# Kernel tuning notes

Measured on AMD Instinct MI355X. Metric: run time of the kernel, lower is better.

The kernel has to match this reference:

```python
import jax, jax.numpy as jnp
import numpy as np

NUM_LEVELS = 16
BASE_RES = 16
DESIRED_RES = 512
EMBED_C = 2
LOG2_HASHMAP = 19
N_POINTS = 262144


def _level_params():
    # torch-ngp gridencoder math, align_corners=True
    S = np.log2(DESIRED_RES / BASE_RES) / (NUM_LEVELS - 1)
    scales = np.exp2(np.arange(NUM_LEVELS) * S) * BASE_RES - 1.0  # float per-level scale
    res = np.ceil(scales).astype(np.int64) + 1                     # per-level grid resolution
    sizes = np.minimum(res ** 3, 2 ** LOG2_HASHMAP)
    sizes = ((sizes + 7) // 8) * 8                                 # round up to multiple of 8
    offsets = np.concatenate([[0], np.cumsum(sizes)])
    return scales.astype(np.float32), res.astype(np.int32), offsets.astype(np.int32)


_CORNERS = np.array([[(c >> d) & 1 for d in range(3)] for c in range(8)], dtype=np.int32)  # [8,3]


def _grid_encode(x, table):
    # x: [N,3] in [0,1]; table: [total_entries, EMBED_C]
    scales, res, offsets = _level_params()
    scales_j = jnp.asarray(scales)[:, None, None]                    # [L,1,1]
    res_j = jnp.asarray(res)[:, None, None]                          # [L,1,1]
    hsize = jnp.asarray(offsets[1:] - offsets[:-1])[:, None, None]   # [L,1,1]
    off = jnp.asarray(offsets[:-1])[:, None, None]                   # [L,1,1]
    pos = x[None, :, :] * scales_j                                   # [L,N,3]
    pos_floor = jnp.floor(pos)
    frac = pos - pos_floor                                           # [L,N,3]
    base = pos_floor.astype(jnp.int32)                               # [L,N,3]
    stride = jnp.concatenate([jnp.ones_like(res_j), res_j, res_j * res_j], axis=-1)  # [L,1,3]
    corners = jnp.asarray(_CORNERS)                                  # [8,3]
    cg = base[:, :, None, :] + corners[None, None]                   # [L,N,8,3]
    w = jnp.where(corners[None, None].astype(bool), frac[:, :, None, :], 1.0 - frac[:, :, None, :])
    w = w[..., 0] * w[..., 1] * w[..., 2]                            # [L,N,8] trilinear weights
    lin = jnp.sum(cg * stride[:, :, None, :], axis=-1)               # [L,N,8] linear corner index
    idx = off + lin % hsize                                          # tiled gridtype: modulo, no hash
    feats = table[idx]                                               # [L,N,8,C] gather
    out = jnp.einsum('lnk,lnkc->lnc', w, feats)                      # [L,N,C]
    n = out.shape[1]
    return out.transpose(1, 0, 2).reshape(n, NUM_LEVELS * EMBED_C)   # [N, L*C]


def setup_inputs() -> dict:
    key = jax.random.key(0)
    ks = jax.random.split(key, 8)
    _, _, offsets = _level_params()
    total = int(offsets[-1])
    inputcoords = jax.random.uniform(ks[0], (N_POINTS, 1, 3), dtype=jnp.float32)  # in [0,1): (x+1)/2 stays in [0,1]
    embeddings = jax.random.normal(ks[1], (total, 1, EMBED_C), dtype=jnp.float32) * 1e-2
    d_in = NUM_LEVELS * EMBED_C  # 32
    W0 = jax.random.normal(ks[2], (d_in, 32), dtype=jnp.float32) / np.sqrt(d_in)
    b0 = jnp.zeros((32,), jnp.float32)
    W1 = jax.random.normal(ks[3], (32, 32), dtype=jnp.float32) / np.sqrt(32.0)
    b1 = jnp.zeros((32,), jnp.float32)
    W2 = jax.random.normal(ks[4], (32, 1), dtype=jnp.float32) / np.sqrt(32.0)
    b2 = jnp.zeros((1,), jnp.float32)
    return {"inputcoords": inputcoords, "embeddings": embeddings,
            "W0": W0, "b0": b0, "W1": W1, "b1": b1, "W2": W2, "b2": b2}


def reference(inputcoords, embeddings, W0, b0, W1, b1, W2, b2):
    bound = 1.0
    x = ((inputcoords + bound) / (2.0 * bound)).reshape(-1, 3)       # [N,3]
    enc = _grid_encode(x, embeddings[:, 0])                          # [N, 32]
    h = enc.reshape(-1, 1, NUM_LEVELS * EMBED_C)                     # [N,1,32]
    h = jax.nn.leaky_relu(h @ W0 + b0, 0.01)
    h = jax.nn.leaky_relu(h @ W1 + b1, 0.01)
    return h @ W2 + b2                                               # [N,1,1]
```

## Files before the change

### kernel.cpp

```cpp
#include <hip/hip_runtime.h>

#define NLVL 16
#define NPTS_PER_BLOCK 256

constexpr float SCALEC[NLVL] = {
    15.0f, 19.15873679831797f, 24.39841683149119f, 31.0f,
    39.31747359663594f, 49.79683366298238f, 63.0f, 79.63494719327189f,
    100.59366732596477f, 127.0f, 160.26989438654376f, 202.18733465192954f,
    255.0f, 321.5397887730875f, 405.3746693038591f, 511.0f
};
constexpr int RESC[NLVL] = {
    16, 21, 26, 32, 41, 51, 64, 81, 102, 128, 162, 204, 256, 323, 407, 512
};
constexpr int OFFC[NLVL] = {
    0, 4096, 13360, 30936, 63704, 132632, 265288, 527432,
    1051720, 1576008, 2100296, 2624584, 3148872, 3673160, 4197448, 4721736
};
constexpr int HMASK = 0x7FFFF;

template<int L>
__device__ __forceinline__ void level_issue(float x, float y, float z,
                                            const float* __restrict__ emb,
                                            float4& q00, float4& q10,
                                            float4& q01, float4& q11,
                                            int& wmask)
{
    constexpr float s = SCALEC[L];
    constexpr int   r = RESC[L];
    constexpr int   off = OFFC[L];

    const float px = x * s, py = y * s, pz = z * s;
    const int bx = (int)floorf(px), by = (int)floorf(py), bz = (int)floorf(pz);
    const int lin = bx + r * by + r * r * bz;

    int i00 = lin, i10 = lin + r, i01 = lin + r * r, i11 = lin + r * r + r;
    if constexpr (L >= 7) {
        i00 &= HMASK; i10 &= HMASK; i01 &= HMASK; i11 &= HMASK;
        wmask = (i00 == HMASK ? 1 : 0) | (i10 == HMASK ? 2 : 0)
              | (i01 == HMASK ? 4 : 0) | (i11 == HMASK ? 8 : 0);
    } else {
        wmask = 0;
    }
    __builtin_memcpy(&q00, emb + 2 * (off + i00), 16);
    __builtin_memcpy(&q10, emb + 2 * (off + i10), 16);
    __builtin_memcpy(&q01, emb + 2 * (off + i01), 16);
    __builtin_memcpy(&q11, emb + 2 * (off + i11), 16);
}

template<int L>
__device__ __forceinline__ void level_accum(float x, float y, float z,
                                            const float* __restrict__ emb,
                                            float4 q00, float4 q10,
                                            float4 q01, float4 q11,
                                            int wmask,
                                            float* __restrict__ h0,
                                            const float* __restrict__ W0)
{
    constexpr float s = SCALEC[L];
    constexpr int   off = OFFC[L];

    const float px = x * s, py = y * s, pz = z * s;
    const float tx = px - floorf(px), ty = py - floorf(py), tz = pz - floorf(pz);

    if constexpr (L >= 7) {
        const float f0x = emb[2 * off], f0y = emb[2 * off + 1];
        q00.z = (wmask & 1) ? f0x : q00.z;  q00.w = (wmask & 1) ? f0y : q00.w;
        q10.z = (wmask & 2) ? f0x : q10.z;  q10.w = (wmask & 2) ? f0y : q10.w;
        q01.z = (wmask & 4) ? f0x : q01.z;  q01.w = (wmask & 4) ? f0y : q01.w;
        q11.z = (wmask & 8) ? f0x : q11.z;  q11.w = (wmask & 8) ? f0y : q11.w;
    }

    const float wx1 = tx, wx0 = 1.0f - tx;
    const float wy1 = ty, wy0 = 1.0f - ty;
    const float wz1 = tz, wz0 = 1.0f - tz;
    const float w00 = wy0 * wz0, w10 = wy1 * wz0;
    const float w01 = wy0 * wz1, w11 = wy1 * wz1;
    float a0 = 0.0f, a1 = 0.0f;
    a0 = fmaf(w00 * wx0, q00.x, a0); a1 = fmaf(w00 * wx0, q00.y, a1);
    a0 = fmaf(w00 * wx1, q00.z, a0); a1 = fmaf(w00 * wx1, q00.w, a1);
    a0 = fmaf(w10 * wx0, q10.x, a0); a1 = fmaf(w10 * wx0, q10.y, a1);
    a0 = fmaf(w10 * wx1, q10.z, a0); a1 = fmaf(w10 * wx1, q10.w, a1);
    a0 = fmaf(w01 * wx0, q01.x, a0); a1 = fmaf(w01 * wx0, q01.y, a1);
    a0 = fmaf(w01 * wx1, q01.z, a0); a1 = fmaf(w01 * wx1, q01.w, a1);
    a0 = fmaf(w11 * wx0, q11.x, a0); a1 = fmaf(w11 * wx0, q11.y, a1);
    a0 = fmaf(w11 * wx1, q11.z, a0); a1 = fmaf(w11 * wx1, q11.w, a1);

#pragma unroll
    for (int j = 0; j < 32; ++j)
        h0[j] = fmaf(a0, W0[(2 * L + 0) * 32 + j], h0[j]);
#pragma unroll
    for (int j = 0; j < 32; ++j)
        h0[j] = fmaf(a1, W0[(2 * L + 1) * 32 + j], h0[j]);
}

__global__ __launch_bounds__(NPTS_PER_BLOCK, 4)
void hashgrid_mlp_kernel(const float* __restrict__ coords,
                         const float* __restrict__ emb,
                         const float* __restrict__ W0,
                         const float* __restrict__ b0,
                         const float* __restrict__ W1,
                         const float* __restrict__ b1,
                         const float* __restrict__ W2,
                         const float* __restrict__ b2,
                         float* __restrict__ out,
                         int n)
{
    const int tid = blockIdx.x * blockDim.x + threadIdx.x;
    if (tid >= n) return;

    const float x = (coords[tid * 3 + 0] + 1.0f) * 0.5f;
    const float y = (coords[tid * 3 + 1] + 1.0f) * 0.5f;
    const float z = (coords[tid * 3 + 2] + 1.0f) * 0.5f;

    float h0[32];
#pragma unroll
    for (int j = 0; j < 32; ++j) h0[j] = b0[j];

    float4 a00, a10, a01, a11; int am;
    float4 b00, b10, b01, b11; int bm;
    float4 c00, c10, c01, c11; int cm;
    float4 d00, d10, d01, d11; int dm;

#define ISS(S, L) level_issue<L>(x, y, z, emb, S##00, S##10, S##01, S##11, S##m);
#define ACC(S, L) level_accum<L>(x, y, z, emb, S##00, S##10, S##01, S##11, S##m, h0, W0);

    ISS(a, 0) ISS(b, 1) ISS(c, 2) ISS(d, 3)
    ACC(a, 0)  ISS(a, 4)
    ACC(b, 1)  ISS(b, 5)
    ACC(c, 2)  ISS(c, 6)
    ACC(d, 3)  ISS(d, 7)
    ACC(a, 4)  ISS(a, 8)
    ACC(b, 5)  ISS(b, 9)
    ACC(c, 6)  ISS(c, 10)
    ACC(d, 7)  ISS(d, 11)
    ACC(a, 8)  ISS(a, 12)
    ACC(b, 9)  ISS(b, 13)
    ACC(c, 10) ISS(c, 14)
    ACC(d, 11) ISS(d, 15)
    ACC(a, 12)
    ACC(b, 13)
    ACC(c, 14)
    ACC(d, 15)

#undef ISS
#undef ACC

#pragma unroll
    for (int j = 0; j < 32; ++j) h0[j] = (h0[j] >= 0.0f) ? h0[j] : 0.01f * h0[j];

    float h1[32];
#pragma unroll
    for (int j = 0; j < 32; ++j) h1[j] = b1[j];
#pragma unroll
    for (int i = 0; i < 32; ++i) {
        const float e = h0[i];
#pragma unroll
        for (int j = 0; j < 32; ++j) h1[j] = fmaf(e, W1[i * 32 + j], h1[j]);
    }
#pragma unroll
    for (int j = 0; j < 32; ++j) h1[j] = (h1[j] >= 0.0f) ? h1[j] : 0.01f * h1[j];

    float acc = b2[0];
#pragma unroll
    for (int j = 0; j < 32; ++j) acc = fmaf(h1[j], W2[j], acc);

    out[tid] = acc;
}

extern "C" void kernel_launch(void* const* d_in, const int* in_sizes, int n_in,
                              void* d_out, int out_size, void* d_ws, size_t ws_size,
                              hipStream_t stream) {
    const float* coords = (const float*)d_in[0];
    const float* emb    = (const float*)d_in[1];
    const float* W0     = (const float*)d_in[2];
    const float* b0     = (const float*)d_in[3];
    const float* W1     = (const float*)d_in[4];
    const float* b1     = (const float*)d_in[5];
    const float* W2     = (const float*)d_in[6];
    const float* b2     = (const float*)d_in[7];
    float* out = (float*)d_out;

    const int n = in_sizes[0] / 3;
    const int blocks = (n + NPTS_PER_BLOCK - 1) / NPTS_PER_BLOCK;
    hashgrid_mlp_kernel<<<blocks, NPTS_PER_BLOCK, 0, stream>>>(
        coords, emb, W0, b0, W1, b1, W2, b2, out, n);
}
```

Before: 98.71 us.

## Issue embedding gathers via inline asm with explicit vmcnt waits for prefetch

Replaces the compiler-generated embedding loads with inline global_load_dwordx4 instructions and inserts explicit s_waitcnt vmcnt counters plus sched barriers. The goal is to keep four levels of gathers in flight, since the compiler might otherwise serialize the loads or wait too early. It risks correctness problems: the level_accum path also issues loads (emb[2*off] and W0 reads) that the compiler does not count, so the hand-set vmcnt values may not match. The sched barriers also restrict instruction scheduling.

After: 133.0 us. 34.8% more time.

```diff
diff --git a/kernel.cpp b/kernel.cpp
--- a/kernel.cpp
+++ b/kernel.cpp
@@ -1,4 +1,6 @@
 #include <hip/hip_runtime.h>
+
+typedef __attribute__((ext_vector_type(4))) float f32x4;
 
 #define NLVL 16
 #define NPTS_PER_BLOCK 256
@@ -21,8 +23,8 @@
 template<int L>
 __device__ __forceinline__ void level_issue(float x, float y, float z,
                                             const float* __restrict__ emb,
-                                            float4& q00, float4& q10,
-                                            float4& q01, float4& q11,
+                                            f32x4& q0, f32x4& q1,
+                                            f32x4& q2, f32x4& q3,
                                             int& wmask)
 {
     constexpr float s = SCALEC[L];
@@ -30,28 +32,31 @@
     constexpr int   off = OFFC[L];
 
     const float px = x * s, py = y * s, pz = z * s;
-    const int bx = (int)floorf(px), by = (int)floorf(py), bz = (int)floorf(pz);
-    const int lin = bx + r * by + r * r * bz;
-
-    int i00 = lin, i10 = lin + r, i01 = lin + r * r, i11 = lin + r * r + r;
+    const int lin = (int)floorf(px) + r * (int)floorf(py) + r * r * (int)floorf(pz);
+
+    int i0 = lin, i1 = lin + r, i2 = lin + r * r, i3 = lin + r * r + r;
     if constexpr (L >= 7) {
-        i00 &= HMASK; i10 &= HMASK; i01 &= HMASK; i11 &= HMASK;
-        wmask = (i00 == HMASK ? 1 : 0) | (i10 == HMASK ? 2 : 0)
-              | (i01 == HMASK ? 4 : 0) | (i11 == HMASK ? 8 : 0);
+        i0 &= HMASK; i1 &= HMASK; i2 &= HMASK; i3 &= HMASK;
+        wmask = (i0 == HMASK ? 1 : 0) | (i1 == HMASK ? 2 : 0)
+              | (i2 == HMASK ? 4 : 0) | (i3 == HMASK ? 8 : 0);
     } else {
         wmask = 0;
     }
-    __builtin_memcpy(&q00, emb + 2 * (off + i00), 16);
-    __builtin_memcpy(&q10, emb + 2 * (off + i10), 16);
-    __builtin_memcpy(&q01, emb + 2 * (off + i01), 16);
-    __builtin_memcpy(&q11, emb + 2 * (off + i11), 16);
+    const float* p0 = emb + 2 * (off + i0);
+    const float* p1 = emb + 2 * (off + i1);
+    const float* p2 = emb + 2 * (off + i2);
+    const float* p3 = emb + 2 * (off + i3);
+    asm volatile("global_load_dwordx4 %0, %1, off" : "=v"(q0) : "v"(p0));
+    asm volatile("global_load_dwordx4 %0, %1, off" : "=v"(q1) : "v"(p1));
+    asm volatile("global_load_dwordx4 %0, %1, off" : "=v"(q2) : "v"(p2));
+    asm volatile("global_load_dwordx4 %0, %1, off" : "=v"(q3) : "v"(p3));
 }
 
 template<int L>
 __device__ __forceinline__ void level_accum(float x, float y, float z,
                                             const float* __restrict__ emb,
-                                            float4 q00, float4 q10,
-                                            float4 q01, float4 q11,
+                                            f32x4 q0, f32x4 q1,
+                                            f32x4 q2, f32x4 q3,
                                             int wmask,
                                             float* __restrict__ h0,
                                             const float* __restrict__ W0)
@@ -64,10 +69,10 @@
 
     if constexpr (L >= 7) {
         const float f0x = emb[2 * off], f0y = emb[2 * off + 1];
-        q00.z = (wmask & 1) ? f0x : q00.z;  q00.w = (wmask & 1) ? f0y : q00.w;
-        q10.z = (wmask & 2) ? f0x : q10.z;  q10.w = (wmask & 2) ? f0y : q10.w;
-        q01.z = (wmask & 4) ? f0x : q01.z;  q01.w = (wmask & 4) ? f0y : q01.w;
-        q11.z = (wmask & 8) ? f0x : q11.z;  q11.w = (wmask & 8) ? f0y : q11.w;
+        q0.z = (wmask & 1) ? f0x : q0.z;  q0.w = (wmask & 1) ? f0y : q0.w;
+        q1.z = (wmask & 2) ? f0x : q1.z;  q1.w = (wmask & 2) ? f0y : q1.w;
+        q2.z = (wmask & 4) ? f0x : q2.z;  q2.w = (wmask & 4) ? f0y : q2.w;
+        q3.z = (wmask & 8) ? f0x : q3.z;  q3.w = (wmask & 8) ? f0y : q3.w;
     }
 
     const float wx1 = tx, wx0 = 1.0f - tx;
@@ -76,14 +81,14 @@
     const float w00 = wy0 * wz0, w10 = wy1 * wz0;
     const float w01 = wy0 * wz1, w11 = wy1 * wz1;
     float a0 = 0.0f, a1 = 0.0f;
-    a0 = fmaf(w00 * wx0, q00.x, a0); a1 = fmaf(w00 * wx0, q00.y, a1);
-    a0 = fmaf(w00 * wx1, q00.z, a0); a1 = fmaf(w00 * wx1, q00.w, a1);
-    a0 = fmaf(w10 * wx0, q10.x, a0); a1 = fmaf(w10 * wx0, q10.y, a1);
-    a0 = fmaf(w10 * wx1, q10.z, a0); a1 = fmaf(w10 * wx1, q10.w, a1);
-    a0 = fmaf(w01 * wx0, q01.x, a0); a1 = fmaf(w01 * wx0, q01.y, a1);
-    a0 = fmaf(w01 * wx1, q01.z, a0); a1 = fmaf(w01 * wx1, q01.w, a1);
-    a0 = fmaf(w11 * wx0, q11.x, a0); a1 = fmaf(w11 * wx0, q11.y, a1);
-    a0 = fmaf(w11 * wx1, q11.z, a0); a1 = fmaf(w11 * wx1, q11.w, a1);
+    a0 = fmaf(w00 * wx0, q0.x, a0); a1 = fmaf(w00 * wx0, q0.y, a1);
+    a0 = fmaf(w00 * wx1, q0.z, a0); a1 = fmaf(w00 * wx1, q0.w, a1);
+    a0 = fmaf(w10 * wx0, q1.x, a0); a1 = fmaf(w10 * wx0, q1.y, a1);
+    a0 = fmaf(w10 * wx1, q1.z, a0); a1 = fmaf(w10 * wx1, q1.w, a1);
+    a0 = fmaf(w01 * wx0, q2.x, a0); a1 = fmaf(w01 * wx0, q2.y, a1);
+    a0 = fmaf(w01 * wx1, q2.z, a0); a1 = fmaf(w01 * wx1, q2.w, a1);
+    a0 = fmaf(w11 * wx0, q3.x, a0); a1 = fmaf(w11 * wx0, q3.y, a1);
+    a0 = fmaf(w11 * wx1, q3.z, a0); a1 = fmaf(w11 * wx1, q3.w, a1);
 
 #pragma unroll
     for (int j = 0; j < 32; ++j)
@@ -116,34 +121,49 @@
 #pragma unroll
     for (int j = 0; j < 32; ++j) h0[j] = b0[j];
 
-    float4 a00, a10, a01, a11; int am;
-    float4 b00, b10, b01, b11; int bm;
-    float4 c00, c10, c01, c11; int cm;
-    float4 d00, d10, d01, d11; int dm;
-
-#define ISS(S, L) level_issue<L>(x, y, z, emb, S##00, S##10, S##01, S##11, S##m);
-#define ACC(S, L) level_accum<L>(x, y, z, emb, S##00, S##10, S##01, S##11, S##m, h0, W0);
-
-    ISS(a, 0) ISS(b, 1) ISS(c, 2) ISS(d, 3)
-    ACC(a, 0)  ISS(a, 4)
-    ACC(b, 1)  ISS(b, 5)
-    ACC(c, 2)  ISS(c, 6)
-    ACC(d, 3)  ISS(d, 7)
-    ACC(a, 4)  ISS(a, 8)
-    ACC(b, 5)  ISS(b, 9)
-    ACC(c, 6)  ISS(c, 10)
-    ACC(d, 7)  ISS(d, 11)
-    ACC(a, 8)  ISS(a, 12)
-    ACC(b, 9)  ISS(b, 13)
-    ACC(c, 10) ISS(c, 14)
-    ACC(d, 11) ISS(d, 15)
-    ACC(a, 12)
-    ACC(b, 13)
-    ACC(c, 14)
-    ACC(d, 15)
-
-#undef ISS
-#undef ACC
+    f32x4 a0, a1, a2, a3; int am;
+    f32x4 b0r, b1r, b2r, b3r; int bm;
+    f32x4 c0, c1, c2, c3; int cm;
+    f32x4 d0, d1, d2, d3; int dm;
+
+#define ISS_A(L) level_issue<L>(x, y, z, emb, a0, a1, a2, a3, am);
+#define ISS_B(L) level_issue<L>(x, y, z, emb, b0r, b1r, b2r, b3r, bm);
+#define ISS_C(L) level_issue<L>(x, y, z, emb, c0, c1, c2, c3, cm);
+#define ISS_D(L) level_issue<L>(x, y, z, emb, d0, d1, d2, d3, dm);
+#define ACC_A(L) level_accum<L>(x, y, z, emb, a0, a1, a2, a3, am, h0, W0);
+#define ACC_B(L) level_accum<L>(x, y, z, emb, b0r, b1r, b2r, b3r, bm, h0, W0);
+#define ACC_C(L) level_accum<L>(x, y, z, emb, c0, c1, c2, c3, cm, h0, W0);
+#define ACC_D(L) level_accum<L>(x, y, z, emb, d0, d1, d2, d3, dm, h0, W0);
+#define VMWAIT(N) asm volatile("s_waitcnt vmcnt(" #N ")" ::: "memory"); \
+                  __builtin_amdgcn_sched_barrier(0);
+
+    ISS_A(0) ISS_B(1) ISS_C(2) ISS_D(3)
+    VMWAIT(12) ACC_A(0)  ISS_A(4)
+    VMWAIT(12) ACC_B(1)  ISS_B(5)
+    VMWAIT(12) ACC_C(2)  ISS_C(6)
+    VMWAIT(12) ACC_D(3)  ISS_D(7)
+    VMWAIT(12) ACC_A(4)  ISS_A(8)
+    VMWAIT(12) ACC_B(5)  ISS_B(9)
+    VMWAIT(12) ACC_C(6)  ISS_C(10)
+    VMWAIT(12) ACC_D(7)  ISS_D(11)
+    VMWAIT(12) ACC_A(8)  ISS_A(12)
+    VMWAIT(12) ACC_B(9)  ISS_B(13)
+    VMWAIT(12) ACC_C(10) ISS_C(14)
+    VMWAIT(12) ACC_D(11) ISS_D(15)
+    VMWAIT(12) ACC_A(12)
+    VMWAIT(8)  ACC_B(13)
+    VMWAIT(4)  ACC_C(14)
+    VMWAIT(0)  ACC_D(15)
+
+#undef ISS_A
+#undef ISS_B
+#undef ISS_C
+#undef ISS_D
+#undef ACC_A
+#undef ACC_B
+#undef ACC_C
+#undef ACC_D
+#undef VMWAIT
 
 #pragma unroll
     for (int j = 0; j < 32; ++j) h0[j] = (h0[j] >= 0.0f) ? h0[j] : 0.01f * h0[j];
```
